# Kernel tuning notes

Hardware: AMD Instinct MI355X
Metric: run time of the kernel (lower is better)

Reference implementation:

```python
import jax, jax.numpy as jnp
import numpy as np

GAMMA = 1.0
BIG = 1e30  # finite stand-in for +inf to keep gradients NaN-free


def pairwise_sqdist(x, y):
    # x: [B, C, N], y: [B, C, M] -> [B, N, M] squared euclidean distances
    xx = jnp.sum(x * x, axis=1)                      # [B, N]
    yy = jnp.sum(y * y, axis=1)                      # [B, M]
    xy = jnp.einsum('bcn,bcm->bnm', x, y)            # [B, N, M]
    return xx[:, :, None] + yy[:, None, :] - 2.0 * xy


def soft_dtw(D, gamma):
    # Anti-diagonal wavefront soft-DTW DP.
    # R[i, j] = D[i-1, j-1] + softmin(R[i-1,j-1], R[i-1,j], R[i,j-1])
    # Diagonal d = i + j; store diag as [B, N+1] arrays indexed by i.
    B, N, M = D.shape
    i_idx = jnp.arange(N + 1)
    # d = 0 diagonal: R[0,0] = 0, everything else +inf
    diag0 = jnp.full((B, N + 1), BIG, D.dtype).at[:, 0].set(0.0)
    # d = 1 diagonal: R[1,0] and R[0,1] are +inf
    diag1 = jnp.full((B, N + 1), BIG, D.dtype)

    def step(carry, d):
        prev2, prev1 = carry                      # diagonals d-2, d-1
        j = d - i_idx                             # 1-based column index
        valid = (i_idx >= 1) & (i_idx <= N) & (j >= 1) & (j <= M)
        di = jnp.clip(i_idx - 1, 0, N - 1)
        dj = jnp.clip(j - 1, 0, M - 1)
        dvals = D[:, di, dj]                      # [B, N+1]
        r0 = jnp.roll(prev2, 1, axis=1)           # R[i-1, j-1]
        r1 = jnp.roll(prev1, 1, axis=1)           # R[i-1, j]
        r2 = prev1                                # R[i, j-1]
        stacked = jnp.stack([r0, r1, r2], axis=0)  # [3, B, N+1]
        softmin = -gamma * jax.nn.logsumexp(-stacked / gamma, axis=0)
        cur = jnp.where(valid[None, :], dvals + softmin, BIG)
        return (prev1, cur), None

    ds = jnp.arange(2, N + M + 1)
    (_, last), _ = jax.lax.scan(step, (diag0, diag1), ds)
    return last[:, N]                             # R[N, M] per batch


def setup_inputs() -> dict:
    key = jax.random.key(0)
    kx, ky = jax.random.split(key)
    B, C, N = 32, 80, 512
    x = jax.random.normal(kx, (B, C, N), dtype=jnp.float32)
    y = jax.random.normal(ky, (B, C, N), dtype=jnp.float32)
    return {"x": x, "y": y}


def reference(x, y):
    D = pairwise_sqdist(x, y)     # save_memory=True path
    return soft_dtw(D, GAMMA)     # [B], normalize=False; squeeze(0) is a no-op
```

## Files before the change

### kernel.cpp

```cpp
#include <hip/hip_runtime.h>
#include <hip/hip_bf16.h>

#define BIGF 1e30f
#define TC 80
#define TN 512
#define L2E 1.4426950408889634f
#define LN2 0.6931471805599453f

typedef float f32x2 __attribute__((ext_vector_type(2)));
typedef float f32x4 __attribute__((ext_vector_type(4)));
typedef short s16x8 __attribute__((ext_vector_type(8)));
typedef __attribute__((address_space(1))) const unsigned int gu32;
typedef __attribute__((address_space(3))) unsigned int lu32;

__global__ __launch_bounds__(256) void pairdist_kernel(
    const float* __restrict__ x, const float* __restrict__ y,
    float* __restrict__ F) {
  const int b  = blockIdx.z;
  const int n0 = blockIdx.x * 128;
  const int m0 = blockIdx.y * 128;

  __shared__ __align__(16) short Ab[128 * 128];
  __shared__ __align__(16) short Bb[128 * 128];
  __shared__ float xxs[128], yys[128];

  const float* xb = x + (size_t)b * TC * TN;
  const float* yb = y + (size_t)b * TC * TN;
  const int tid = threadIdx.x;

  auto sw = [](int row, int k) -> int {
    return (row * 256 + k * 2) ^ ((row & 7) << 4);
  };
  auto cvt = [](float f) -> unsigned short {
    unsigned u = __float_as_uint(f);
    return (unsigned short)((u + 0x7FFFu + ((u >> 16) & 1u)) >> 16);
  };

  for (int item = tid; item < 12 * 128 * 2; item += 256) {
    int arr = (item >= 12 * 128) ? 1 : 0;
    int it  = item - arr * 12 * 128;
    int oct = it >> 7, n = it & 127;
    const float* src = arr ? (yb + m0 + n) : (xb + n0 + n);
    s16x8 pk;
#pragma unroll
    for (int j = 0; j < 8; ++j) {
      int c = oct * 8 + j;
      float v = (c < TC) ? src[(size_t)c * TN] : 0.f;
      pk[j] = (short)cvt(v);
    }
    short* dst = arr ? Bb : Ab;
    *(s16x8*)((char*)dst + sw(n, oct * 8)) = pk;
  }

  if (tid < 128) {
    float s = 0.f;
    for (int c = 0; c < TC; ++c) {
      float v = xb[(size_t)c * TN + n0 + tid];
      s += v * v;
    }
    xxs[tid] = s;
  } else {
    int n = tid - 128;
    float s = 0.f;
    for (int c = 0; c < TC; ++c) {
      float v = yb[(size_t)c * TN + m0 + n];
      s += v * v;
    }
    yys[n] = s;
  }
  __syncthreads();

  const int l  = tid & 63;
  const int w  = tid >> 6;
  const int wm = (w >> 1) * 64, wn = (w & 1) * 64;
  const int fr = l & 15;
  const int fk = (l >> 4) * 8;

  f32x4 acc[4][4] = {};
#pragma unroll
  for (int ks = 0; ks < 3; ++ks) {
    const int k0 = ks * 32 + fk;
    s16x8 af[4], bfr[4];
#pragma unroll
    for (int ta = 0; ta < 4; ++ta)
      af[ta] = *(const s16x8*)((const char*)Ab + sw(wm + ta * 16 + fr, k0));
#pragma unroll
    for (int tq = 0; tq < 4; ++tq)
      bfr[tq] = *(const s16x8*)((const char*)Bb + sw(wn + tq * 16 + fr, k0));
#pragma unroll
    for (int ta = 0; ta < 4; ++ta)
#pragma unroll
      for (int tq = 0; tq < 4; ++tq)
        acc[ta][tq] = __builtin_amdgcn_mfma_f32_16x16x32_bf16(
            af[ta], bfr[tq], acc[ta][tq], 0, 0, 0);
  }

  float* Fb = F + (size_t)b * TN * TN;
#pragma unroll
  for (int ta = 0; ta < 4; ++ta) {
    const int mb = wm + ta * 16 + (l >> 4) * 4;
#pragma unroll
    for (int r = 0; r < 4; ++r) {
      const int jj = n0 + mb + r;
      const float xxv = xxs[mb + r];
#pragma unroll
      for (int tq = 0; tq < 4; ++tq) {
        const int nn = wn + tq * 16 + fr;
        const int i  = m0 + nn;
        float val = (xxv + yys[nn] - 2.f * acc[ta][tq][r]) * L2E;
        int p = (jj + (i >> 1)) & (TN - 1);
        Fb[(size_t)p * TN + i] = val;
      }
    }
  }
}

__global__ __launch_bounds__(256) __attribute__((amdgpu_waves_per_eu(1)))
void sdtw_kernel(const float* __restrict__ Ft, float* __restrict__ out) {
  const int b   = blockIdx.x;
  const int tid = threadIdx.x;
  const int g   = tid & 63;
  const int w   = tid >> 6;
  const float* Fb = Ft + (size_t)b * TN * TN;

  __shared__ float ring[4][8][128];
  __shared__ f32x4 hand[3][2][2];

  if (tid < 12) {
    f32x4 iv; iv[0] = BIGF; iv[1] = BIGF; iv[2] = BIGF; iv[3] = BIGF;
    ((f32x4*)hand)[tid] = iv;
  }
  __syncthreads();

  float p0 = BIGF, p1 = BIGF;
  float up_p = (tid == 0) ? 0.f : BIGF;

  auto stage = [&](int slot, int u) {
    const float* gp =
        Fb + (size_t)((u - 7 * w) & (TN - 1)) * TN + w * 128 + g;
    __builtin_amdgcn_global_load_lds((gu32*)gp,        (lu32*)&ring[w][slot][0],  4, 0, 0);
    __builtin_amdgcn_global_load_lds((gu32*)(gp + 64), (lu32*)&ring[w][slot][64], 4, 0, 0);
  };

  const unsigned rbase =
      (unsigned)(size_t)(__attribute__((address_space(3))) float*)&ring[w][0][0];
  const unsigned hbase =
      (unsigned)(size_t)(__attribute__((address_space(3))) f32x4*)&hand[0][0];

  auto cell = [&](float d, float r0, float r1, float r2) -> float {
    float mn, md, mx;
    asm("v_min3_f32 %0, %3, %4, %5\n\t"
        "v_med3_f32 %1, %3, %4, %5\n\t"
        "v_max3_f32 %2, %3, %4, %5"
        : "=&v"(mn), "=&v"(md), "=&v"(mx)
        : "v"(r0), "v"(r1), "v"(r2));
    float e1 = __builtin_amdgcn_exp2f(mn - md);
    float e2 = __builtin_amdgcn_exp2f(mn - mx);
    float dm = d + mn;
    float ss = (1.0f + e1) + e2;
    return dm - __builtin_amdgcn_logf(ss);
  };

  auto body = [&](f32x2 d, float pubk) -> float {
    float upc = __int_as_float(__builtin_amdgcn_update_dpp(
        __float_as_int(pubk), __float_as_int(p1), 0x138, 0xf, 0xf, false));
    float c0 = cell(d[0], up_p, upc, p0);
    float c1 = cell(d[1], p0, c0, p1);
    p0 = c0; p1 = c1; up_p = upc;
    return c1;
  };

  stage(0, 0); stage(1, 1); stage(2, 2); stage(3, 3);
  stage(4, 4); stage(5, 5); stage(6, 6); stage(7, 7);

  f32x2 d0, d1, d2, d3, d4, d5, d6, d7;

  int s = 0;
  for (int B = 0; B < 98; ++B, s += 8) {
    __builtin_amdgcn_s_barrier();
    asm volatile("s_waitcnt vmcnt(0)" ::: "memory");

    unsigned ad = rbase + (unsigned)(g * 8);
    asm volatile(
        "ds_read_b64 %0, %8\n\t"
        "ds_read_b64 %1, %8 offset:512\n\t"
        "ds_read_b64 %2, %8 offset:1024\n\t"
        "ds_read_b64 %3, %8 offset:1536\n\t"
        "ds_read_b64 %4, %8 offset:2048\n\t"
        "ds_read_b64 %5, %8 offset:2560\n\t"
        "ds_read_b64 %6, %8 offset:3072\n\t"
        "ds_read_b64 %7, %8 offset:3584\n\t"
        "s_waitcnt lgkmcnt(0)"
        : "=&v"(d0), "=&v"(d1), "=&v"(d2), "=&v"(d3),
          "=&v"(d4), "=&v"(d5), "=&v"(d6), "=&v"(d7)
        : "v"(ad)
        : "memory");

    f32x4 pA, pB;
    if (w > 0) {
      unsigned ha = hbase + (unsigned)(((w - 1) * 2 + ((B + 1) & 1)) * 32);
      asm volatile("ds_read_b128 %0, %2\n\t"
                   "ds_read_b128 %1, %2 offset:16\n\t"
                   "s_waitcnt lgkmcnt(0)"
                   : "=&v"(pA), "=&v"(pB) : "v"(ha) : "memory");
    } else {
      pA[0] = pA[1] = pA[2] = pA[3] = BIGF;
      pB[0] = pB[1] = pB[2] = pB[3] = BIGF;
    }

    stage(0, s + 8);  stage(1, s + 9);
    stage(2, s + 10); stage(3, s + 11);
    stage(4, s + 12); stage(5, s + 13);
    stage(6, s + 14); stage(7, s + 15);

    f32x4 k0, k1;
    k0[0] = body(d0, pA[0]); k0[1] = body(d1, pA[1]);
    k0[2] = body(d2, pA[2]); k0[3] = body(d3, pA[3]);
    k1[0] = body(d4, pB[0]); k1[1] = body(d5, pB[1]);
    k1[2] = body(d6, pB[2]); k1[3] = body(d7, pB[3]);

    if (w < 3 && g == 63) {
      unsigned wa = hbase + (unsigned)((w * 2 + (B & 1)) * 32);
      asm volatile("ds_write_b128 %0, %1\n\t"
                   "ds_write_b128 %0, %2 offset:16\n\t"
                   "s_waitcnt lgkmcnt(0)"
                   :: "v"(wa), "v"(k0), "v"(k1) : "memory");
    }
  }

  __builtin_amdgcn_s_barrier();
  asm volatile("s_waitcnt vmcnt(0)" ::: "memory");
  {
    unsigned ad = rbase + (unsigned)(g * 8);
    asm volatile(
        "ds_read_b64 %0, %4\n\t"
        "ds_read_b64 %1, %4 offset:512\n\t"
        "ds_read_b64 %2, %4 offset:1024\n\t"
        "ds_read_b64 %3, %4 offset:1536\n\t"
        "s_waitcnt lgkmcnt(0)"
        : "=&v"(d0), "=&v"(d1), "=&v"(d2), "=&v"(d3)
        : "v"(ad)
        : "memory");
  }
  f32x4 pA;
  if (w > 0) {
    unsigned ha = hbase + (unsigned)(((w - 1) * 2 + 1) * 32);
    asm volatile("ds_read_b128 %0, %1\n\ts_waitcnt lgkmcnt(0)"
                 : "=&v"(pA) : "v"(ha) : "memory");
  } else {
    pA[0] = pA[1] = pA[2] = pA[3] = BIGF;
  }
  body(d0, pA[0]); body(d1, pA[1]); body(d2, pA[2]); body(d3, pA[3]);

  if (tid == 255) out[b] = p1 * LN2;
}

extern "C" void kernel_launch(void* const* d_in, const int* in_sizes, int n_in,
                              void* d_out, int out_size, void* d_ws, size_t ws_size,
                              hipStream_t stream) {
  const float* x = (const float*)d_in[0];
  const float* y = (const float*)d_in[1];
  float* out = (float*)d_out;
  float* F = (float*)d_ws;

  dim3 g1(TN / 128, TN / 128, 32);
  pairdist_kernel<<<g1, 256, 0, stream>>>(y, x, F);
  sdtw_kernel<<<32, 256, 0, stream>>>(F, out);
}
```

Baseline: 177.2 us.

## Split soft-DTW wavefront across 8 waves with one row per lane

The soft-DTW kernel now uses 512 threads (8 waves), each lane owning one DP row instead of two, and the diagonal skew in the distance layout changes to match. The serial chain per lane halves in length, but the pipeline gains more wave-to-wave handoff stages and a longer total step count (134 blocks instead of 98 plus a tail). The trade is shorter per-step dependency work against more pipeline fill latency and barrier traffic across 8 waves.

Result: slower. 216.5 us (+22.2%).

```diff
diff --git a/kernel.cpp b/kernel.cpp
--- a/kernel.cpp
+++ b/kernel.cpp
@@ -108,14 +108,14 @@
         const int nn = wn + tq * 16 + fr;
         const int i  = m0 + nn;
         float val = (xxv + yys[nn] - 2.f * acc[ta][tq][r]) * L2E;
-        int p = (jj + (i >> 1)) & (TN - 1);
+        int p = (jj + i) & (TN - 1);
         Fb[(size_t)p * TN + i] = val;
       }
     }
   }
 }
 
-__global__ __launch_bounds__(256) __attribute__((amdgpu_waves_per_eu(1)))
+__global__ __launch_bounds__(512) __attribute__((amdgpu_waves_per_eu(2)))
 void sdtw_kernel(const float* __restrict__ Ft, float* __restrict__ out) {
   const int b   = blockIdx.x;
   const int tid = threadIdx.x;
@@ -123,29 +123,29 @@
   const int w   = tid >> 6;
   const float* Fb = Ft + (size_t)b * TN * TN;
 
-  __shared__ float ring[4][8][128];
-  __shared__ f32x4 hand[3][2][2];
-
-  if (tid < 12) {
+  __shared__ float ring[8][8][64];
+  __shared__ f32x4 hand[7][2][2];
+
+  if (tid < 28) {
     f32x4 iv; iv[0] = BIGF; iv[1] = BIGF; iv[2] = BIGF; iv[3] = BIGF;
     ((f32x4*)hand)[tid] = iv;
   }
   __syncthreads();
 
-  float p0 = BIGF, p1 = BIGF;
+  float p    = BIGF;
   float up_p = (tid == 0) ? 0.f : BIGF;
 
   auto stage = [&](int slot, int u) {
     const float* gp =
-        Fb + (size_t)((u - 7 * w) & (TN - 1)) * TN + w * 128 + g;
-    __builtin_amdgcn_global_load_lds((gu32*)gp,        (lu32*)&ring[w][slot][0],  4, 0, 0);
-    __builtin_amdgcn_global_load_lds((gu32*)(gp + 64), (lu32*)&ring[w][slot][64], 4, 0, 0);
+        Fb + (size_t)((u - 7 * w) & (TN - 1)) * TN + w * 64 + g;
+    __builtin_amdgcn_global_load_lds((gu32*)gp, (lu32*)&ring[w][slot][0],
+                                     4, 0, 0);
   };
 
   const unsigned rbase =
       (unsigned)(size_t)(__attribute__((address_space(3))) float*)&ring[w][0][0];
   const unsigned hbase =
-      (unsigned)(size_t)(__attribute__((address_space(3))) f32x4*)&hand[0][0];
+      (unsigned)(size_t)(__attribute__((address_space(3))) f32x4*)&hand[0][0][0];
 
   auto cell = [&](float d, float r0, float r1, float r2) -> float {
     float mn, md, mx;
@@ -161,35 +161,34 @@
     return dm - __builtin_amdgcn_logf(ss);
   };
 
-  auto body = [&](f32x2 d, float pubk) -> float {
+  auto body = [&](float d, float pubk) -> float {
     float upc = __int_as_float(__builtin_amdgcn_update_dpp(
-        __float_as_int(pubk), __float_as_int(p1), 0x138, 0xf, 0xf, false));
-    float c0 = cell(d[0], up_p, upc, p0);
-    float c1 = cell(d[1], p0, c0, p1);
-    p0 = c0; p1 = c1; up_p = upc;
-    return c1;
+        __float_as_int(pubk), __float_as_int(p), 0x138, 0xf, 0xf, false));
+    float cur = cell(d, up_p, upc, p);
+    up_p = upc; p = cur;
+    return cur;
   };
 
   stage(0, 0); stage(1, 1); stage(2, 2); stage(3, 3);
   stage(4, 4); stage(5, 5); stage(6, 6); stage(7, 7);
 
-  f32x2 d0, d1, d2, d3, d4, d5, d6, d7;
+  float d0, d1, d2, d3, d4, d5, d6, d7;
 
   int s = 0;
-  for (int B = 0; B < 98; ++B, s += 8) {
+  for (int B = 0; B < 134; ++B, s += 8) {
     __builtin_amdgcn_s_barrier();
     asm volatile("s_waitcnt vmcnt(0)" ::: "memory");
 
-    unsigned ad = rbase + (unsigned)(g * 8);
+    unsigned ad = rbase + (unsigned)(g * 4);
     asm volatile(
-        "ds_read_b64 %0, %8\n\t"
-        "ds_read_b64 %1, %8 offset:512\n\t"
-        "ds_read_b64 %2, %8 offset:1024\n\t"
-        "ds_read_b64 %3, %8 offset:1536\n\t"
-        "ds_read_b64 %4, %8 offset:2048\n\t"
-        "ds_read_b64 %5, %8 offset:2560\n\t"
-        "ds_read_b64 %6, %8 offset:3072\n\t"
-        "ds_read_b64 %7, %8 offset:3584\n\t"
+        "ds_read_b32 %0, %8\n\t"
+        "ds_read_b32 %1, %8 offset:256\n\t"
+        "ds_read_b32 %2, %8 offset:512\n\t"
+        "ds_read_b32 %3, %8 offset:768\n\t"
+        "ds_read_b32 %4, %8 offset:1024\n\t"
+        "ds_read_b32 %5, %8 offset:1280\n\t"
+        "ds_read_b32 %6, %8 offset:1536\n\t"
+        "ds_read_b32 %7, %8 offset:1792\n\t"
         "s_waitcnt lgkmcnt(0)"
         : "=&v"(d0), "=&v"(d1), "=&v"(d2), "=&v"(d3),
           "=&v"(d4), "=&v"(d5), "=&v"(d6), "=&v"(d7)
@@ -219,7 +218,7 @@
     k1[0] = body(d4, pB[0]); k1[1] = body(d5, pB[1]);
     k1[2] = body(d6, pB[2]); k1[3] = body(d7, pB[3]);
 
-    if (w < 3 && g == 63) {
+    if (w < 7 && g == 63) {
       unsigned wa = hbase + (unsigned)((w * 2 + (B & 1)) * 32);
       asm volatile("ds_write_b128 %0, %1\n\t"
                    "ds_write_b128 %0, %2 offset:16\n\t"
@@ -228,31 +227,7 @@
     }
   }
 
-  __builtin_amdgcn_s_barrier();
-  asm volatile("s_waitcnt vmcnt(0)" ::: "memory");
-  {
-    unsigned ad = rbase + (unsigned)(g * 8);
-    asm volatile(
-        "ds_read_b64 %0, %4\n\t"
-        "ds_read_b64 %1, %4 offset:512\n\t"
-        "ds_read_b64 %2, %4 offset:1024\n\t"
-        "ds_read_b64 %3, %4 offset:1536\n\t"
-        "s_waitcnt lgkmcnt(0)"
-        : "=&v"(d0), "=&v"(d1), "=&v"(d2), "=&v"(d3)
-        : "v"(ad)
-        : "memory");
-  }
-  f32x4 pA;
-  if (w > 0) {
-    unsigned ha = hbase + (unsigned)(((w - 1) * 2 + 1) * 32);
-    asm volatile("ds_read_b128 %0, %1\n\ts_waitcnt lgkmcnt(0)"
-                 : "=&v"(pA) : "v"(ha) : "memory");
-  } else {
-    pA[0] = pA[1] = pA[2] = pA[3] = BIGF;
-  }
-  body(d0, pA[0]); body(d1, pA[1]); body(d2, pA[2]); body(d3, pA[3]);
-
-  if (tid == 255) out[b] = p1 * LN2;
+  if (w == 7 && g == 63) out[b] = p * LN2;
 }
 
 extern "C" void kernel_launch(void* const* d_in, const int* in_sizes, int n_in,
@@ -265,5 +240,5 @@
 
   dim3 g1(TN / 128, TN / 128, 32);
   pairdist_kernel<<<g1, 256, 0, stream>>>(y, x, F);
-  sdtw_kernel<<<32, 256, 0, stream>>>(F, out);
+  sdtw_kernel<<<32, 512, 0, stream>>>(F, out);
 }
```
